# Performance work log

Measured on AMD Instinct MI355X. Metric: run time of the kernel, lower is better.

## Reference

```python
import jax, jax.numpy as jnp
import numpy as np
import math

D = 2048
NH = 16       # query heads
NKV = 4       # kv heads (GQA)
HD = 128
SOFTCLAMP = 50.0
ROPE_BASE = 10000.0
B = 4
SQ_VLM = 1024
SQ_ACT = 64
S_CACHE = 256


def _heads(x, n):
    # [B,S,n*HD] -> [B,n,S,HD]
    b, s, _ = x.shape
    return x.reshape(b, s, n, HD).transpose(0, 2, 1, 3)


def _rope_cos_sin(pos):
    # pos: [B,S] int -> cos,sin [B,1,S,HD]
    inv_freq = 1.0 / (ROPE_BASE ** (jnp.arange(0, HD, 2, dtype=jnp.float32) / HD))
    freqs = pos.astype(jnp.float32)[..., None] * inv_freq  # [B,S,HD/2]
    emb = jnp.concatenate([freqs, freqs], axis=-1)         # [B,S,HD]
    return jnp.cos(emb)[:, None], jnp.sin(emb)[:, None]


def _apply_rope(x, cos, sin):
    # x: [B,H,S,HD]
    x1, x2 = x[..., : HD // 2], x[..., HD // 2 :]
    rot = jnp.concatenate([-x2, x1], axis=-1)
    return x * cos + rot * sin


def setup_inputs() -> dict:
    key = jax.random.key(0)
    ks = jax.random.split(key, 16)
    sc = lambda d: 1.0 / math.sqrt(d)
    inp = {
        'attention_mask': jnp.zeros((B, 1, SQ_VLM + SQ_ACT, S_CACHE + SQ_VLM + SQ_ACT), jnp.float32),
        'pos_vlm': jnp.broadcast_to(jnp.arange(S_CACHE, S_CACHE + SQ_VLM, dtype=jnp.int32), (B, SQ_VLM)),
        'pos_action': jnp.broadcast_to(jnp.arange(S_CACHE + SQ_VLM, S_CACHE + SQ_VLM + SQ_ACT, dtype=jnp.int32), (B, SQ_ACT)),
        'h_vlm': jax.random.normal(ks[0], (B, SQ_VLM, D), jnp.float32),
        'h_action': jax.random.normal(ks[1], (B, SQ_ACT, D), jnp.float32),
        'k_cache': jax.random.normal(ks[2], (B, NKV, S_CACHE, HD), jnp.float32),
        'v_cache': jax.random.normal(ks[3], (B, NKV, S_CACHE, HD), jnp.float32),
        'Wq_vlm': jax.random.normal(ks[4], (D, NH * HD), jnp.float32) * sc(D),
        'Wk_vlm': jax.random.normal(ks[5], (D, NKV * HD), jnp.float32) * sc(D),
        'Wv_vlm': jax.random.normal(ks[6], (D, NKV * HD), jnp.float32) * sc(D),
        'Wq_act': jax.random.normal(ks[7], (D, NH * HD), jnp.float32) * sc(D),
        'Wk_act': jax.random.normal(ks[8], (D, NKV * HD), jnp.float32) * sc(D),
        'Wv_act': jax.random.normal(ks[9], (D, NKV * HD), jnp.float32) * sc(D),
        'Wo_act': jax.random.normal(ks[10], (NH * HD, D), jnp.float32) * sc(NH * HD),
    }
    return inp


def reference(attention_mask, pos_vlm, pos_action, h_vlm, h_action, k_cache, v_cache,
              Wq_vlm, Wk_vlm, Wv_vlm, Wq_act, Wk_act, Wv_act, Wo_act):
    group = NH // NKV

    def qkv(h, pos, Wq, Wk, Wv):
        q = _heads(h @ Wq, NH)
        k = _heads(h @ Wk, NKV)
        v = _heads(h @ Wv, NKV)
        cos, sin = _rope_cos_sin(pos)
        return _apply_rope(q, cos, sin), _apply_rope(k, cos, sin), v

    q_v, k_v, v_v = qkv(h_vlm, pos_vlm, Wq_vlm, Wk_vlm, Wv_vlm)
    q_a, k_a, v_a = qkv(h_action, pos_action, Wq_act, Wk_act, Wv_act)

    # repeat_kv (GQA) on every KV source, cached mixture first (append_non_active order)
    rep = lambda t: jnp.repeat(t, group, axis=1)  # [B,NKV,S,HD] -> [B,NH,S,HD]
    k = jnp.concatenate([rep(k_cache), rep(k_v), rep(k_a)], axis=2)
    v = jnp.concatenate([rep(v_cache), rep(v_v), rep(v_a)], axis=2)
    q = jnp.concatenate([q_v, q_a], axis=2)  # [B,NH,Sq,HD]

    scores = jnp.einsum('bhqd,bhkd->bhqk', q, k) / math.sqrt(HD)
    scores = jnp.tanh(scores / SOFTCLAMP) * SOFTCLAMP + attention_mask
    w = jax.nn.softmax(scores.astype(jnp.float32), axis=-1).astype(q.dtype)
    out = jnp.einsum('bhqk,bhkd->bhqd', w, v)
    out = out.transpose(0, 2, 1, 3).reshape(B, SQ_VLM + SQ_ACT, NH * HD)

    # split by q_lens; 'vlm' is in post_attn_skip_names -> no o_proj, dropped
    out_action = out[:, SQ_VLM:, :]
    return out_action @ Wo_act
```

## Files before the change

### kernel.cpp

```cpp
#include <hip/hip_runtime.h>
#include <cmath>

#define NH 16
#define NKV 4
#define HD 128
#define DMODEL 2048
#define BB 4
#define SQV 1024
#define SQA 64
#define SCACHE 256
#define STOT 1344
#define SQTOT 1088
#define NSPLIT 7

typedef unsigned short u16;
typedef __attribute__((ext_vector_type(8))) short short8;
typedef __attribute__((ext_vector_type(4))) float f32x4;

__device__ __forceinline__ float b2f(u16 u) {
    union { float f; unsigned int i; } x; x.i = ((unsigned int)u) << 16; return x.f;
}
__device__ __forceinline__ u16 f2b(float f) {
    unsigned int x = __float_as_uint(f);
    x = x + 0x7fffu + ((x >> 16) & 1u);
    return (u16)(x >> 16);
}

__device__ __forceinline__ void gload16(const void* g, void* l) {
    __builtin_amdgcn_global_load_lds((const __attribute__((address_space(1))) void*)g,
                                     (__attribute__((address_space(3))) void*)l, 16, 0, 0);
}

__device__ __forceinline__ void transpose_body(const float* in, u16* out, int N,
                                               int bx, int by) {
    __shared__ __align__(16) u16 t[64 * 66];
    int n0 = bx * 64, k0 = by * 64;
    int tid = threadIdx.x;
    int r = tid >> 3;
    int c8 = (tid & 7) * 8;
#pragma unroll
    for (int h = 0; h < 2; h++) {
        int k = r + h * 32;
        const float* f = in + (size_t)(k0 + k) * N + n0 + c8;
        float4 a = *(const float4*)f, b = *(const float4*)(f + 4);
        u16 vv[8] = {f2b(a.x), f2b(a.y), f2b(a.z), f2b(a.w),
                     f2b(b.x), f2b(b.y), f2b(b.z), f2b(b.w)};
#pragma unroll
        for (int j = 0; j < 8; j++) t[(c8 + j) * 66 + k] = vv[j];
    }
    __syncthreads();
#pragma unroll
    for (int h = 0; h < 2; h++) {
        int n = r + h * 32;
        short8 v;
#pragma unroll
        for (int j = 0; j < 8; j++) ((u16*)&v)[j] = t[n * 66 + c8 + j];
        *(short8*)(out + (size_t)(n0 + n) * 2048 + k0 + c8) = v;
    }
}

__device__ __forceinline__ void transpose_vc(const float* vc, u16* VT, int idx) {
    __shared__ __align__(16) u16 tv[64 * 66];
    int bkv = idx >> 3, t8 = idx & 7;
    int key0 = (t8 >> 1) * 64, d0 = (t8 & 1) * 64;
    const float* in = vc + ((size_t)bkv * SCACHE + key0) * HD + d0;
    u16* out = VT + ((size_t)bkv * HD + d0) * STOT + key0;
    int tid = threadIdx.x;
    int r = tid >> 3, c8 = (tid & 7) * 8;
#pragma unroll
    for (int h = 0; h < 2; h++) {
        int k = r + h * 32;
        const float* f = in + (size_t)k * HD + c8;
        float4 a = *(const float4*)f, b = *(const float4*)(f + 4);
        u16 vv[8] = {f2b(a.x), f2b(a.y), f2b(a.z), f2b(a.w),
                     f2b(b.x), f2b(b.y), f2b(b.z), f2b(b.w)};
#pragma unroll
        for (int j = 0; j < 8; j++) tv[(c8 + j) * 66 + k] = vv[j];
    }
    __syncthreads();
#pragma unroll
    for (int h = 0; h < 2; h++) {
        int d = r + h * 32;
        short8 v;
#pragma unroll
        for (int j = 0; j < 8; j++) ((u16*)&v)[j] = tv[d * 66 + c8 + j];
        *(short8*)(out + (size_t)d * STOT + c8) = v;
    }
}

__global__ void k_prep(const float* __restrict__ mask,
                       const float* __restrict__ kc, const float* __restrict__ vc,
                       const float* __restrict__ hv, const float* __restrict__ ha,
                       const float* __restrict__ w0, u16* __restrict__ o0,
                       const float* __restrict__ w1, u16* __restrict__ o1,
                       const float* __restrict__ w2, u16* __restrict__ o2,
                       const float* __restrict__ w3, u16* __restrict__ o3,
                       const float* __restrict__ w4, u16* __restrict__ o4,
                       const float* __restrict__ w5, u16* __restrict__ o5,
                       float* __restrict__ cosT, float* __restrict__ sinT,
                       u16* __restrict__ maskS, u16* __restrict__ K_all, u16* __restrict__ VT_all,
                       u16* __restrict__ hv16, u16* __restrict__ ha16) {
    int gx = blockIdx.x, tid = threadIdx.x;
    if (gx < 3072) {
        if (gx < 256)        transpose_body(w0, o0, 512,  gx & 7,  gx >> 3);
        else if (gx < 512)   { int g = gx - 256;  transpose_body(w1, o1, 512,  g & 7,  g >> 3); }
        else if (gx < 768)   { int g = gx - 512;  transpose_body(w2, o2, 512,  g & 7,  g >> 3); }
        else if (gx < 1024)  { int g = gx - 768;  transpose_body(w3, o3, 512,  g & 7,  g >> 3); }
        else if (gx < 2048)  { int g = gx - 1024; transpose_body(w4, o4, 2048, g & 31, g >> 5); }
        else                 { int g = gx - 2048; transpose_body(w5, o5, 2048, g & 31, g >> 5); }
        return;
    }
    int bx = gx - 3072;
    if (bx < 336) {
        int i = bx * 256 + tid;
        if (i < STOT * 64) {
            int p = i >> 6, j = i & 63;
            float inv = __expf(-(float)j * (9.210340371976184f / 64.0f));
            float ang = (float)p * inv;
            cosT[i] = cosf(ang);
            sinT[i] = sinf(ang);
        }
    } else if (bx < 1680) {
        int i = (bx - 336) * 256 + tid;
        int b = i / (SQA * STOT);
        int r = i % (SQA * STOT);
        size_t s = (size_t)b * SQTOT * STOT + (size_t)SQV * STOT + r;
        maskS[i] = f2b(mask[s]);
    } else if (bx < 1936) {
        int i = (bx - 1680) * 256 + tid;
        int e = i * 8;
        int bk = e / (SCACHE * HD);
        int off = e % (SCACHE * HD);
        size_t dst = (size_t)bk * STOT * HD + off;
        const float* fk = kc + e;
        u16 tk[8];
#pragma unroll
        for (int j = 0; j < 8; j++) tk[j] = f2b(fk[j]);
        *(short8*)(K_all + dst) = *(short8*)tk;
    } else if (bx < 6032) {
        int i = (bx - 1936) * 256 + tid;
        int e = i * 8;
        const float* f = hv + e;
        float4 a = *(const float4*)f, b = *(const float4*)(f + 4);
        u16 t[8] = {f2b(a.x), f2b(a.y), f2b(a.z), f2b(a.w),
                    f2b(b.x), f2b(b.y), f2b(b.z), f2b(b.w)};
        *(short8*)(hv16 + e) = *(short8*)t;
    } else if (bx < 6288) {
        int i = (bx - 6032) * 256 + tid;
        int e = i * 8;
        const float* f = ha + e;
        float4 a = *(const float4*)f, b = *(const float4*)(f + 4);
        u16 t[8] = {f2b(a.x), f2b(a.y), f2b(a.z), f2b(a.w),
                    f2b(b.x), f2b(b.y), f2b(b.z), f2b(b.w)};
        *(short8*)(ha16 + e) = *(short8*)t;
    } else {
        transpose_vc(vc, VT_all, bx - 6288);
    }
}

__global__ __launch_bounds__(256) void k_gemm_qkv(
    const u16* __restrict__ Avlm, const u16* __restrict__ Aact,
    const u16* __restrict__ WkvT, const u16* __restrict__ WvvT,
    const u16* __restrict__ WqaT, const u16* __restrict__ WkaT, const u16* __restrict__ WvaT,
    const int* __restrict__ pos_vlm, const int* __restrict__ pos_act,
    const float* __restrict__ cosT, const float* __restrict__ sinT,
    u16* __restrict__ Qbuf, u16* __restrict__ K_all, u16* __restrict__ VT_all) {
    __shared__ __align__(16) u16 smem[3 * 12288];
    int tid = threadIdx.x;
    int w = tid >> 6, lane = tid & 63;
    int la = lane & 15, lg = lane >> 4;
    int wm = (w & 1) * 32;
    int c2 = w >> 1;
    int ntab[4] = {c2 * 2, c2 * 2 + 1, c2 * 2 + 4, c2 * 2 + 5};

    const u16* A; const u16* Bt; int m0, n0;
    int path;
    int head;
    int bid = blockIdx.x;
    if (bid < 512) {
        m0 = (bid & 63) * 64;
        int yy = bid >> 6;
        path = (yy < 4) ? 0 : 1;
        head = yy & 3;
        n0 = head * 128;
        A = Avlm;
        Bt = (path == 0) ? WkvT : WvvT;
    } else {
        int g = bid - 512;
        m0 = (g & 3) * 64;
        int ny = g >> 2;
        A = Aact;
        if (ny < 16)      { path = 2; head = ny;      Bt = WqaT; n0 = ny * 128; }
        else if (ny < 20) { path = 3; head = ny - 16; Bt = WkaT; n0 = (ny - 16) * 128; }
        else              { path = 4; head = ny - 20; Bt = WvaT; n0 = (ny - 20) * 128; }
    }

    f32x4 acc[2][4];
#pragma unroll
    for (int i = 0; i < 2; i++)
#pragma unroll
        for (int j = 0; j < 4; j++) acc[i][j] = (f32x4){0.f, 0.f, 0.f, 0.f};

    int srow = tid >> 3;
    int scsrc = (((tid & 7) * 16) ^ ((srow & 7) << 4)) >> 1;

#define STAGE_QKV(BASE, KB) do {                                                      \
        u16* Ab_ = (BASE);                                                            \
        u16* Bb_ = Ab_ + 4096;                                                        \
        _Pragma("unroll")                                                             \
        for (int h = 0; h < 2; h++)                                                   \
            gload16(A + (size_t)(m0 + srow + h * 32) * DMODEL + (KB) + scsrc,         \
                    Ab_ + h * 2048 + tid * 8);                                        \
        _Pragma("unroll")                                                             \
        for (int h = 0; h < 4; h++)                                                   \
            gload16(Bt + (size_t)(n0 + srow + h * 32) * DMODEL + (KB) + scsrc,        \
                    Bb_ + h * 2048 + tid * 8);                                        \
    } while (0)

    STAGE_QKV(smem, 0);
    STAGE_QKV(smem + 12288, 64);
    int bufR = 0, bufS = 2;
    int swr = (la & 7) << 3;
    for (int t = 0; t < 32; ++t) {
        if (t < 31) asm volatile("s_waitcnt vmcnt(6)" ::: "memory");
        else        asm volatile("s_waitcnt vmcnt(0)" ::: "memory");
        __builtin_amdgcn_s_barrier();
        asm volatile("" ::: "memory");
        if (t < 30) STAGE_QKV(smem + bufS * 12288, (t + 2) * 64);
        const u16* Ac = smem + bufR * 12288;
        const u16* Bc = Ac + 4096;
#pragma unroll
        for (int kk = 0; kk < 2; kk++) {
            short8 af[2], bf[4];
            int cc = (kk * 32 + lg * 8) ^ swr;
#pragma unroll
            for (int mt = 0; mt < 2; mt++)
                af[mt] = *(const short8*)&Ac[(wm + mt * 16 + la) * 64 + cc];
#pragma unroll
            for (int nt = 0; nt < 4; nt++)
                bf[nt] = *(const short8*)&Bc[(ntab[nt] * 16 + la) * 64 + cc];
#pragma unroll
            for (int mt = 0; mt < 2; mt++)
#pragma unroll
                for (int nt = 0; nt < 4; nt++)
                    acc[mt][nt] = __builtin_amdgcn_mfma_f32_16x16x32_bf16(af[mt], bf[nt], acc[mt][nt], 0, 0, 0);
        }
        bufR = (bufR == 2) ? 0 : bufR + 1;
        bufS = (bufS == 2) ? 0 : bufS + 1;
    }
#undef STAGE_QKV

#pragma unroll
    for (int mt = 0; mt < 2; mt++) {
#pragma unroll
        for (int r = 0; r < 4; r++) {
            int gm = m0 + wm + mt * 16 + lg * 4 + r;
            if (path <= 1) {
                int b = gm >> 10, s = gm & 1023;
                if (path == 0) {
                    size_t base = ((size_t)(b * NKV + head) * STOT + SCACHE + s) * HD;
                    int pos = pos_vlm[gm];
#pragma unroll
                    for (int i = 0; i < 2; i++) {
                        int dlo = ntab[i] * 16 + la;
                        float x1 = acc[mt][i][r], x2 = acc[mt][i + 2][r];
                        float cs = cosT[pos * 64 + dlo], sn = sinT[pos * 64 + dlo];
                        K_all[base + dlo]      = f2b(x1 * cs - x2 * sn);
                        K_all[base + dlo + 64] = f2b(x2 * cs + x1 * sn);
                    }
                } else {
                    size_t vt = ((size_t)(b * NKV + head) * HD) * STOT + SCACHE + s;
#pragma unroll
                    for (int i = 0; i < 4; i++) {
                        int d = ntab[i] * 16 + la;
                        VT_all[vt + (size_t)d * STOT] = f2b(acc[mt][i][r]);
                    }
                }
            } else {
                int b = gm >> 6, s = gm & 63;
                if (path == 2) {
                    int pos = pos_act[gm];
                    size_t qb = ((size_t)(b * NH + head) * SQA + s) * HD;
#pragma unroll
                    for (int i = 0; i < 2; i++) {
                        int dlo = ntab[i] * 16 + la;
                        float x1 = acc[mt][i][r], x2 = acc[mt][i + 2][r];
                        float cs = cosT[pos * 64 + dlo], sn = sinT[pos * 64 + dlo];
                        Qbuf[qb + dlo]      = f2b(x1 * cs - x2 * sn);
                        Qbuf[qb + dlo + 64] = f2b(x2 * cs + x1 * sn);
                    }
                } else if (path == 3) {
                    int pos = pos_act[gm];
                    size_t base = ((size_t)(b * NKV + head) * STOT + SCACHE + SQV + s) * HD;
#pragma unroll
                    for (int i = 0; i < 2; i++) {
                        int dlo = ntab[i] * 16 + la;
                        float x1 = acc[mt][i][r], x2 = acc[mt][i + 2][r];
                        float cs = cosT[pos * 64 + dlo], sn = sinT[pos * 64 + dlo];
                        K_all[base + dlo]      = f2b(x1 * cs - x2 * sn);
                        K_all[base + dlo + 64] = f2b(x2 * cs + x1 * sn);
                    }
                } else {
                    size_t vt = ((size_t)(b * NKV + head) * HD) * STOT + SCACHE + SQV + s;
#pragma unroll
                    for (int i = 0; i < 4; i++) {
                        int d = ntab[i] * 16 + la;
                        VT_all[vt + (size_t)d * STOT] = f2b(acc[mt][i][r]);
                    }
                }
            }
        }
    }
}

__global__ __launch_bounds__(256) void k_attn_split(
    const u16* __restrict__ Qbuf, const u16* __restrict__ K_all, const u16* __restrict__ VT_all,
    const u16* __restrict__ maskS, u16* __restrict__ po, float* __restrict__ pml) {
    int h = blockIdx.x, b = blockIdx.y, p = blockIdx.z;
    int bh = b * NH + h;
    int kvh = h >> 2;
    const u16* Kb  = K_all  + (size_t)(b * NKV + kvh) * STOT * HD;
    const u16* VTb = VT_all + (size_t)(b * NKV + kvh) * HD * STOT;
    const u16* Qb  = Qbuf + (size_t)bh * SQA * HD;
    int tid = threadIdx.x, w = tid >> 6, lane = tid & 63;
    int la = lane & 15, lg = lane >> 4;
    __shared__ __align__(16) u16 Ks[2][64 * 128];
    __shared__ __align__(16) u16 Vt[2][128 * 64];
    __shared__ __align__(16) u16 Ps[4][16 * 72];

    int kr = tid >> 4;
    int ksw = (((tid & 15) * 16) ^ ((kr & 7) << 4)) >> 1;
    int vr = tid >> 3;
    int vsw = (((tid & 7) * 16) ^ ((vr & 7) << 4)) >> 1;

#define ASTAGE(CB, G) do {                                                            \
        _Pragma("unroll")                                                             \
        for (int hh = 0; hh < 4; hh++)                                                \
            gload16(Kb + (size_t)((G) * 64 + kr + hh * 16) * HD + ksw,                \
                    &Ks[CB][hh * 2048 + tid * 8]);                                    \
        _Pragma("unroll")                                                             \
        for (int hh = 0; hh < 4; hh++)                                                \
            gload16(VTb + (size_t)(vr + hh * 32) * STOT + (G) * 64 + vsw,             \
                    &Vt[CB][hh * 2048 + tid * 8]);                                    \
    } while (0)

    ASTAGE(0, p * 3);
    short8 qf[4];
#pragma unroll
    for (int kk = 0; kk < 4; kk++)
        qf[kk] = *(const short8*)(Qb + (size_t)(w * 16 + la) * HD + kk * 32 + lg * 8);
    f32x4 o_acc[8];
#pragma unroll
    for (int nt = 0; nt < 8; nt++) o_acc[nt] = (f32x4){0.f, 0.f, 0.f, 0.f};
    float m_run[4], l_run[4];
#pragma unroll
    for (int r = 0; r < 4; r++) { m_run[r] = -3e38f; l_run[r] = 0.f; }

    int cur = 0;
    int swr = (la & 7) << 3;
    const float scl = 0.08838834764831845f;
    for (int c = 0; c < 3; c++) {
        int g = p * 3 + c;
        u16 mreg[4][4];
#pragma unroll
        for (int nt = 0; nt < 4; nt++)
#pragma unroll
            for (int r = 0; r < 4; r++)
                mreg[nt][r] = maskS[((size_t)(b * SQA + w * 16 + lg * 4 + r)) * STOT +
                                    g * 64 + nt * 16 + la];
        if (c < 2) {
            ASTAGE(cur ^ 1, g + 1);
            asm volatile("s_waitcnt vmcnt(8)" ::: "memory");
        } else {
            asm volatile("s_waitcnt vmcnt(0)" ::: "memory");
        }
        __builtin_amdgcn_s_barrier();
        asm volatile("" ::: "memory");
        f32x4 s_acc[4];
#pragma unroll
        for (int nt = 0; nt < 4; nt++) s_acc[nt] = (f32x4){0.f, 0.f, 0.f, 0.f};
        __builtin_amdgcn_s_setprio(1);
#pragma unroll
        for (int kk = 0; kk < 4; kk++) {
            int cc = (kk * 32 + lg * 8) ^ swr;
#pragma unroll
            for (int nt = 0; nt < 4; nt++) {
                short8 kf = *(const short8*)&Ks[cur][(nt * 16 + la) * 128 + cc];
                s_acc[nt] = __builtin_amdgcn_mfma_f32_16x16x32_bf16(qf[kk], kf, s_acc[nt], 0, 0, 0);
            }
        }
        __builtin_amdgcn_s_setprio(0);
        float sc[4][4];
#pragma unroll
        for (int nt = 0; nt < 4; nt++) {
#pragma unroll
            for (int r = 0; r < 4; r++) {
                float sv = s_acc[nt][r] * scl;
                float x = sv * 0.02f;
                float t = __expf(-2.0f * fabsf(x));
                float th = __fdividef(1.0f - t, 1.0f + t);
                sv = copysignf(th, x) * 50.0f;
                sv += b2f(mreg[nt][r]);
                sc[nt][r] = sv;
            }
        }
#pragma unroll
        for (int r = 0; r < 4; r++) {
            float mx = fmaxf(fmaxf(sc[0][r], sc[1][r]), fmaxf(sc[2][r], sc[3][r]));
#pragma unroll
            for (int sh = 1; sh < 16; sh <<= 1) mx = fmaxf(mx, __shfl_xor(mx, sh, 64));
            if (mx > m_run[r] + 8.0f) {
                float alpha = __expf(m_run[r] - mx);
                m_run[r] = mx;
                l_run[r] *= alpha;
#pragma unroll
                for (int nt = 0; nt < 8; nt++) o_acc[nt][r] *= alpha;
            }
            float rowsum = 0.f;
#pragma unroll
            for (int nt = 0; nt < 4; nt++) {
                float pv = __expf(sc[nt][r] - m_run[r]);
                Ps[w][(lg * 4 + r) * 72 + nt * 16 + la] = f2b(pv);
                rowsum += pv;
            }
#pragma unroll
            for (int sh = 1; sh < 16; sh <<= 1) rowsum += __shfl_xor(rowsum, sh, 64);
            l_run[r] += rowsum;
        }
        __builtin_amdgcn_s_setprio(1);
#pragma unroll
        for (int kk = 0; kk < 2; kk++) {
            short8 pf = *(const short8*)&Ps[w][la * 72 + kk * 32 + lg * 8];
            int cc = (kk * 32 + lg * 8) ^ swr;
#pragma unroll
            for (int nt = 0; nt < 8; nt++) {
                short8 vf = *(const short8*)&Vt[cur][(nt * 16 + la) * 64 + cc];
                o_acc[nt] = __builtin_amdgcn_mfma_f32_16x16x32_bf16(pf, vf, o_acc[nt], 0, 0, 0);
            }
        }
        __builtin_amdgcn_s_setprio(0);
        __builtin_amdgcn_s_barrier();
        cur ^= 1;
    }
#undef ASTAGE
#pragma unroll
    for (int nt = 0; nt < 8; nt++) {
#pragma unroll
        for (int r = 0; r < 4; r++) {
            int sq = w * 16 + lg * 4 + r;
            po[(((size_t)p * 64 + bh) * 64 + sq) * 128 + nt * 16 + la] = f2b(o_acc[nt][r]);
        }
    }
    if (la == 0) {
#pragma unroll
        for (int r = 0; r < 4; r++) {
            int sq = w * 16 + lg * 4 + r;
            size_t mlb = (((size_t)p * 64 + bh) * 64 + sq) * 2;
            pml[mlb] = m_run[r];
            pml[mlb + 1] = l_run[r];
        }
    }
}

__global__ __launch_bounds__(256) void k_attn_red(
    const u16* __restrict__ po, const float* __restrict__ pml, u16* __restrict__ AO) {
    int h = blockIdx.x, b = blockIdx.y, qz = blockIdx.z * 16;
    int bh = b * NH + h;
    __shared__ float wgt[NSPLIT][16];
    int tid = threadIdx.x;
    if (tid < 16) {
        int q = qz + tid;
        float m[NSPLIT], l[NSPLIT], M = -3e38f;
#pragma unroll
        for (int p = 0; p < NSPLIT; p++) {
            size_t mlb = (((size_t)p * 64 + bh) * 64 + q) * 2;
            m[p] = pml[mlb]; l[p] = pml[mlb + 1];
            M = fmaxf(M, m[p]);
        }
        float L = 0.f;
#pragma unroll
        for (int p = 0; p < NSPLIT; p++) L += l[p] * __expf(m[p] - M);
        float inv = 1.0f / L;
#pragma unroll
        for (int p = 0; p < NSPLIT; p++) wgt[p][tid] = __expf(m[p] - M) * inv;
    }
    __syncthreads();
    for (int e = tid; e < 16 * 128; e += 256) {
        int q = qz + (e >> 7), d = e & 127;
        float s = 0.f;
#pragma unroll
        for (int p = 0; p < NSPLIT; p++)
            s += b2f(po[(((size_t)p * 64 + bh) * 64 + q) * 128 + d]) * wgt[p][e >> 7];
        AO[((size_t)(b * SQA + q)) * 2048 + h * HD + d] = f2b(s);
    }
}

__global__ __launch_bounds__(256) void k_gemm_out(
    const u16* __restrict__ A, const u16* __restrict__ WoT, float* __restrict__ out) {
    __shared__ __align__(16) u16 smem[2 * 6144];
    int m0 = blockIdx.x * 32, n0 = blockIdx.y * 64;
    int tid = threadIdx.x;
    int w = tid >> 6, lane = tid & 63;
    int la = lane & 15, lg = lane >> 4;
    int wm = (w & 1) * 16, wn = (w >> 1) * 32;
    f32x4 acc[2];
#pragma unroll
    for (int j = 0; j < 2; j++) acc[j] = (f32x4){0.f, 0.f, 0.f, 0.f};

    int srow = tid >> 3;
    int scsrc = (((tid & 7) * 16) ^ ((srow & 7) << 4)) >> 1;

#define STAGE_OUT(CB, KB) do {                                                        \
        u16* Ab_ = smem + (CB) * 6144;                                                \
        u16* Bb_ = Ab_ + 2048;                                                        \
        gload16(A + (size_t)(m0 + srow) * DMODEL + (KB) + scsrc, Ab_ + tid * 8);      \
        _Pragma("unroll")                                                             \
        for (int h = 0; h < 2; h++)                                                   \
            gload16(WoT + (size_t)(n0 + srow + h * 32) * DMODEL + (KB) + scsrc,       \
                    Bb_ + h * 2048 + tid * 8);                                        \
    } while (0)

    STAGE_OUT(0, 0);
    int cur = 0;
    int swr = (la & 7) << 3;
    for (int kb = 0; kb < DMODEL; kb += 64) {
        if (kb + 64 < DMODEL) {
            STAGE_OUT(cur ^ 1, kb + 64);
            asm volatile("s_waitcnt vmcnt(3)" ::: "memory");
        } else {
            asm volatile("s_waitcnt vmcnt(0)" ::: "memory");
        }
        __builtin_amdgcn_s_barrier();
        asm volatile("" ::: "memory");
        const u16* Ac = smem + cur * 6144;
        const u16* Bc = Ac + 2048;
#pragma unroll
        for (int kk = 0; kk < 2; kk++) {
            int cc = (kk * 32 + lg * 8) ^ swr;
            short8 af = *(const short8*)&Ac[(wm + la) * 64 + cc];
            short8 bf[2];
#pragma unroll
            for (int nt = 0; nt < 2; nt++) bf[nt] = *(const short8*)&Bc[(wn + nt * 16 + la) * 64 + cc];
#pragma unroll
            for (int nt = 0; nt < 2; nt++)
                acc[nt] = __builtin_amdgcn_mfma_f32_16x16x32_bf16(af, bf[nt], acc[nt], 0, 0, 0);
        }
        __builtin_amdgcn_s_barrier();
        cur ^= 1;
    }
#undef STAGE_OUT

#pragma unroll
    for (int r = 0; r < 4; r++) {
        int gm = m0 + wm + lg * 4 + r;
#pragma unroll
        for (int nt = 0; nt < 2; nt++)
            out[(size_t)gm * DMODEL + n0 + wn + nt * 16 + la] = acc[nt][r];
    }
}

extern "C" void kernel_launch(void* const* d_in, const int* in_sizes, int n_in,
                              void* d_out, int out_size, void* d_ws, size_t ws_size,
                              hipStream_t stream) {
    (void)in_sizes; (void)n_in; (void)out_size;
    const float* mask    = (const float*)d_in[0];
    const int*   pos_vlm = (const int*)d_in[1];
    const int*   pos_act = (const int*)d_in[2];
    const float* h_vlm   = (const float*)d_in[3];
    const float* h_act   = (const float*)d_in[4];
    const float* k_cache = (const float*)d_in[5];
    const float* v_cache = (const float*)d_in[6];
    const float* Wk_vlm  = (const float*)d_in[8];
    const float* Wv_vlm  = (const float*)d_in[9];
    const float* Wq_act  = (const float*)d_in[10];
    const float* Wk_act  = (const float*)d_in[11];
    const float* Wv_act  = (const float*)d_in[12];
    const float* Wo_act  = (const float*)d_in[13];

    const size_t NEED = 65273856;
    if (ws_size < NEED) return;
    char* ws = (char*)d_ws;
    float* cosT  = (float*)(ws + 0);
    float* sinT  = (float*)(ws + 344064);
    u16* K_all   = (u16*)(ws + 688128);
    u16* VT_all  = (u16*)(ws + 6193152);
    u16* Qbuf    = (u16*)(ws + 11698176);
    u16* AO      = (u16*)(ws + 12746752);
    u16* WkvT    = (u16*)(ws + 13795328);
    u16* WvvT    = (u16*)(ws + 15892480);
    u16* WqaT    = (u16*)(ws + 17989632);
    u16* WkaT    = (u16*)(ws + 26378240);
    u16* WvaT    = (u16*)(ws + 28475392);
    u16* WoT     = (u16*)(ws + 30572544);
    u16* po      = (u16*)(ws + 38961152);
    float* pml   = (float*)(ws + 46301184);
    u16* maskS   = (u16*)(ws + 46759936);
    u16* hv16    = (u16*)(ws + 47448064);
    u16* ha16    = (u16*)(ws + 64225280);

    hipLaunchKernelGGL(k_prep, dim3(9488), dim3(256), 0, stream,
                       mask, k_cache, v_cache, h_vlm, h_act,
                       Wk_vlm, WkvT, Wv_vlm, WvvT, Wk_act, WkaT, Wv_act, WvaT,
                       Wq_act, WqaT, Wo_act, WoT,
                       cosT, sinT, maskS, K_all, VT_all, hv16, ha16);
    hipLaunchKernelGGL(k_gemm_qkv, dim3(608), dim3(256), 0, stream,
                       hv16, ha16, WkvT, WvvT, WqaT, WkaT, WvaT,
                       pos_vlm, pos_act, cosT, sinT, Qbuf, K_all, VT_all);
    hipLaunchKernelGGL(k_attn_split, dim3(16, 4, NSPLIT), dim3(256), 0, stream,
                       Qbuf, K_all, VT_all, maskS, po, pml);
    hipLaunchKernelGGL(k_attn_red, dim3(16, 4, 4), dim3(256), 0, stream, po, pml, AO);
    hipLaunchKernelGGL(k_gemm_out, dim3(8, 32), dim3(256), 0, stream, AO, WoT, (float*)d_out);
}
```

Measured before the change: 234.4 us.

## Fuse all stages into one cooperative persistent kernel with grid syncs

```diff
diff --git a/kernel.cpp b/kernel.cpp
--- a/kernel.cpp
+++ b/kernel.cpp
@@ -1,5 +1,8 @@
 #include <hip/hip_runtime.h>
+#include <hip/hip_cooperative_groups.h>
 #include <cmath>
+
+namespace cg = cooperative_groups;
 
 #define NH 16
 #define NKV 4
@@ -31,9 +34,24 @@
                                      (__attribute__((address_space(3))) void*)l, 16, 0, 0);
 }
 
-__device__ __forceinline__ void transpose_body(const float* in, u16* out, int N,
+struct MegaArgs {
+    const float *mask, *kc, *vc, *hv, *ha;
+    const float *w0; u16* o0;
+    const float *w1; u16* o1;
+    const float *w2; u16* o2;
+    const float *w3; u16* o3;
+    const float *w4; u16* o4;
+    const float *w5; u16* o5;
+    const int *pos_vlm, *pos_act;
+    float *cosT, *sinT;
+    u16 *maskS, *K_all, *VT_all, *hv16, *ha16, *Qbuf, *po;
+    float* pml;
+    u16* AO;
+    float* out;
+};
+
+__device__ __forceinline__ void transpose_body(u16* t, const float* in, u16* out, int N,
                                                int bx, int by) {
-    __shared__ __align__(16) u16 t[64 * 66];
     int n0 = bx * 64, k0 = by * 64;
     int tid = threadIdx.x;
     int r = tid >> 3;
@@ -59,8 +77,7 @@
     }
 }
 
-__device__ __forceinline__ void transpose_vc(const float* vc, u16* VT, int idx) {
-    __shared__ __align__(16) u16 tv[64 * 66];
+__device__ __forceinline__ void transpose_vc(u16* tv, const float* vc, u16* VT, int idx) {
     int bkv = idx >> 3, t8 = idx & 7;
     int key0 = (t8 >> 1) * 64, d0 = (t8 & 1) * 64;
     const float* in = vc + ((size_t)bkv * SCACHE + key0) * HD + d0;
@@ -88,26 +105,15 @@
     }
 }
 
-__global__ void k_prep(const float* __restrict__ mask,
-                       const float* __restrict__ kc, const float* __restrict__ vc,
-                       const float* __restrict__ hv, const float* __restrict__ ha,
-                       const float* __restrict__ w0, u16* __restrict__ o0,
-                       const float* __restrict__ w1, u16* __restrict__ o1,
-                       const float* __restrict__ w2, u16* __restrict__ o2,
-                       const float* __restrict__ w3, u16* __restrict__ o3,
-                       const float* __restrict__ w4, u16* __restrict__ o4,
-                       const float* __restrict__ w5, u16* __restrict__ o5,
-                       float* __restrict__ cosT, float* __restrict__ sinT,
-                       u16* __restrict__ maskS, u16* __restrict__ K_all, u16* __restrict__ VT_all,
-                       u16* __restrict__ hv16, u16* __restrict__ ha16) {
-    int gx = blockIdx.x, tid = threadIdx.x;
+__device__ __forceinline__ void prep_work(const MegaArgs& a, u16* L, int gx) {
+    int tid = threadIdx.x;
     if (gx < 3072) {
-        if (gx < 256)        transpose_body(w0, o0, 512,  gx & 7,  gx >> 3);
-        else if (gx < 512)   { int g = gx - 256;  transpose_body(w1, o1, 512,  g & 7,  g >> 3); }
-        else if (gx < 768)   { int g = gx - 512;  transpose_body(w2, o2, 512,  g & 7,  g >> 3); }
-        else if (gx < 1024)  { int g = gx - 768;  transpose_body(w3, o3, 512,  g & 7,  g >> 3); }
-        else if (gx < 2048)  { int g = gx - 1024; transpose_body(w4, o4, 2048, g & 31, g >> 5); }
-        else                 { int g = gx - 2048; transpose_body(w5, o5, 2048, g & 31, g >> 5); }
+        if (gx < 256)        transpose_body(L, a.w0, a.o0, 512,  gx & 7,  gx >> 3);
+        else if (gx < 512)   { int g = gx - 256;  transpose_body(L, a.w1, a.o1, 512,  g & 7,  g >> 3); }
+        else if (gx < 768)   { int g = gx - 512;  transpose_body(L, a.w2, a.o2, 512,  g & 7,  g >> 3); }
+        else if (gx < 1024)  { int g = gx - 768;  transpose_body(L, a.w3, a.o3, 512,  g & 7,  g >> 3); }
+        else if (gx < 2048)  { int g = gx - 1024; transpose_body(L, a.w4, a.o4, 2048, g & 31, g >> 5); }
+        else                 { int g = gx - 2048; transpose_body(L, a.w5, a.o5, 2048, g & 31, g >> 5); }
         return;
     }
     int bx = gx - 3072;
@@ -117,55 +123,50 @@
             int p = i >> 6, j = i & 63;
             float inv = __expf(-(float)j * (9.210340371976184f / 64.0f));
             float ang = (float)p * inv;
-            cosT[i] = cosf(ang);
-            sinT[i] = sinf(ang);
+            a.cosT[i] = cosf(ang);
+            a.sinT[i] = sinf(ang);
         }
     } else if (bx < 1680) {
         int i = (bx - 336) * 256 + tid;
         int b = i / (SQA * STOT);
         int r = i % (SQA * STOT);
         size_t s = (size_t)b * SQTOT * STOT + (size_t)SQV * STOT + r;
-        maskS[i] = f2b(mask[s]);
+        a.maskS[i] = f2b(a.mask[s]);
     } else if (bx < 1936) {
         int i = (bx - 1680) * 256 + tid;
         int e = i * 8;
         int bk = e / (SCACHE * HD);
         int off = e % (SCACHE * HD);
         size_t dst = (size_t)bk * STOT * HD + off;
-        const float* fk = kc + e;
+        const float* fk = a.kc + e;
         u16 tk[8];
 #pragma unroll
         for (int j = 0; j < 8; j++) tk[j] = f2b(fk[j]);
-        *(short8*)(K_all + dst) = *(short8*)tk;
+        *(short8*)(a.K_all + dst) = *(short8*)tk;
     } else if (bx < 6032) {
         int i = (bx - 1936) * 256 + tid;
         int e = i * 8;
-        const float* f = hv + e;
-        float4 a = *(const float4*)f, b = *(const float4*)(f + 4);
-        u16 t[8] = {f2b(a.x), f2b(a.y), f2b(a.z), f2b(a.w),
-                    f2b(b.x), f2b(b.y), f2b(b.z), f2b(b.w)};
-        *(short8*)(hv16 + e) = *(short8*)t;
+        const float* f = a.hv + e;
+        float4 p0 = *(const float4*)f, p1 = *(const float4*)(f + 4);
+        u16 t8[8] = {f2b(p0.x), f2b(p0.y), f2b(p0.z), f2b(p0.w),
+                     f2b(p1.x), f2b(p1.y), f2b(p1.z), f2b(p1.w)};
+        *(short8*)(a.hv16 + e) = *(short8*)t8;
     } else if (bx < 6288) {
         int i = (bx - 6032) * 256 + tid;
         int e = i * 8;
-        const float* f = ha + e;
-        float4 a = *(const float4*)f, b = *(const float4*)(f + 4);
-        u16 t[8] = {f2b(a.x), f2b(a.y), f2b(a.z), f2b(a.w),
-                    f2b(b.x), f2b(b.y), f2b(b.z), f2b(b.w)};
-        *(short8*)(ha16 + e) = *(short8*)t;
+        const float* f = a.ha + e;
+        float4 p0 = *(const float4*)f, p1 = *(const float4*)(f + 4);
+        u16 t8[8] = {f2b(p0.x), f2b(p0.y), f2b(p0.z), f2b(p0.w),
+                     f2b(p1.x), f2b(p1.y), f2b(p1.z), f2b(p1.w)};
+        *(short8*)(a.ha16 + e) = *(short8*)t8;
     } else {
-        transpose_vc(vc, VT_all, bx - 6288);
-    }
-}
-
-__global__ __launch_bounds__(256) void k_gemm_qkv(
-    const u16* __restrict__ Avlm, const u16* __restrict__ Aact,
-    const u16* __restrict__ WkvT, const u16* __restrict__ WvvT,
-    const u16* __restrict__ WqaT, const u16* __restrict__ WkaT, const u16* __restrict__ WvaT,
-    const int* __restrict__ pos_vlm, const int* __restrict__ pos_act,
-    const float* __restrict__ cosT, const float* __restrict__ sinT,
-    u16* __restrict__ Qbuf, u16* __restrict__ K_all, u16* __restrict__ VT_all) {
-    __shared__ __align__(16) u16 smem[3 * 12288];
+        transpose_vc(L, a.vc, a.VT_all, bx - 6288);
+    }
+}
+
+__device__ __forceinline__ void qkv_tile(const MegaArgs& a, u16* smem,
+                                         const u16* A, const u16* Bt,
+                                         int m0, int n0, int path, int head) {
     int tid = threadIdx.x;
     int w = tid >> 6, lane = tid & 63;
     int la = lane & 15, lg = lane >> 4;
@@ -173,28 +174,6 @@
     int c2 = w >> 1;
     int ntab[4] = {c2 * 2, c2 * 2 + 1, c2 * 2 + 4, c2 * 2 + 5};
 
-    const u16* A; const u16* Bt; int m0, n0;
-    int path;
-    int head;
-    int bid = blockIdx.x;
-    if (bid < 512) {
-        m0 = (bid & 63) * 64;
-        int yy = bid >> 6;
-        path = (yy < 4) ? 0 : 1;
-        head = yy & 3;
-        n0 = head * 128;
-        A = Avlm;
-        Bt = (path == 0) ? WkvT : WvvT;
-    } else {
-        int g = bid - 512;
-        m0 = (g & 3) * 64;
-        int ny = g >> 2;
-        A = Aact;
-        if (ny < 16)      { path = 2; head = ny;      Bt = WqaT; n0 = ny * 128; }
-        else if (ny < 20) { path = 3; head = ny - 16; Bt = WkaT; n0 = (ny - 16) * 128; }
-        else              { path = 4; head = ny - 20; Bt = WvaT; n0 = (ny - 20) * 128; }
-    }
-
     f32x4 acc[2][4];
 #pragma unroll
     for (int i = 0; i < 2; i++)
@@ -204,8 +183,8 @@
     int srow = tid >> 3;
     int scsrc = (((tid & 7) * 16) ^ ((srow & 7) << 4)) >> 1;
 
-#define STAGE_QKV(BASE, KB) do {                                                      \
-        u16* Ab_ = (BASE);                                                            \
+#define STAGE_QKV(CB, KB) do {                                                        \
+        u16* Ab_ = smem + (CB) * 12288;                                               \
         u16* Bb_ = Ab_ + 4096;                                                        \
         _Pragma("unroll")                                                             \
         for (int h = 0; h < 2; h++)                                                   \
@@ -217,17 +196,19 @@
                     Bb_ + h * 2048 + tid * 8);                                        \
     } while (0)
 
-    STAGE_QKV(smem, 0);
-    STAGE_QKV(smem + 12288, 64);
-    int bufR = 0, bufS = 2;
+    STAGE_QKV(0, 0);
+    int cur = 0;
     int swr = (la & 7) << 3;
-    for (int t = 0; t < 32; ++t) {
-        if (t < 31) asm volatile("s_waitcnt vmcnt(6)" ::: "memory");
-        else        asm volatile("s_waitcnt vmcnt(0)" ::: "memory");
+    for (int kb = 0; kb < DMODEL; kb += 64) {
+        if (kb + 64 < DMODEL) {
+            STAGE_QKV(cur ^ 1, kb + 64);
+            asm volatile("s_waitcnt vmcnt(6)" ::: "memory");
+        } else {
+            asm volatile("s_waitcnt vmcnt(0)" ::: "memory");
+        }
         __builtin_amdgcn_s_barrier();
         asm volatile("" ::: "memory");
-        if (t < 30) STAGE_QKV(smem + bufS * 12288, (t + 2) * 64);
-        const u16* Ac = smem + bufR * 12288;
+        const u16* Ac = smem + cur * 12288;
         const u16* Bc = Ac + 4096;
 #pragma unroll
         for (int kk = 0; kk < 2; kk++) {
@@ -245,8 +226,8 @@
                 for (int nt = 0; nt < 4; nt++)
                     acc[mt][nt] = __builtin_amdgcn_mfma_f32_16x16x32_bf16(af[mt], bf[nt], acc[mt][nt], 0, 0, 0);
         }
-        bufR = (bufR == 2) ? 0 : bufR + 1;
-        bufS = (bufS == 2) ? 0 : bufS + 1;
+        __builtin_amdgcn_s_barrier();
+        cur ^= 1;
     }
 #undef STAGE_QKV
 
@@ -259,53 +240,53 @@
                 int b = gm >> 10, s = gm & 1023;
                 if (path == 0) {
                     size_t base = ((size_t)(b * NKV + head) * STOT + SCACHE + s) * HD;
-                    int pos = pos_vlm[gm];
+                    int pos = a.pos_vlm[gm];
 #pragma unroll
                     for (int i = 0; i < 2; i++) {
                         int dlo = ntab[i] * 16 + la;
                         float x1 = acc[mt][i][r], x2 = acc[mt][i + 2][r];
-                        float cs = cosT[pos * 64 + dlo], sn = sinT[pos * 64 + dlo];
-                        K_all[base + dlo]      = f2b(x1 * cs - x2 * sn);
-                        K_all[base + dlo + 64] = f2b(x2 * cs + x1 * sn);
+                        float cs = a.cosT[pos * 64 + dlo], sn = a.sinT[pos * 64 + dlo];
+                        a.K_all[base + dlo]      = f2b(x1 * cs - x2 * sn);
+                        a.K_all[base + dlo + 64] = f2b(x2 * cs + x1 * sn);
                     }
                 } else {
                     size_t vt = ((size_t)(b * NKV + head) * HD) * STOT + SCACHE + s;
 #pragma unroll
                     for (int i = 0; i < 4; i++) {
                         int d = ntab[i] * 16 + la;
-                        VT_all[vt + (size_t)d * STOT] = f2b(acc[mt][i][r]);
+                        a.VT_all[vt + (size_t)d * STOT] = f2b(acc[mt][i][r]);
                     }
                 }
             } else {
                 int b = gm >> 6, s = gm & 63;
                 if (path == 2) {
-                    int pos = pos_act[gm];
+                    int pos = a.pos_act[gm];
                     size_t qb = ((size_t)(b * NH + head) * SQA + s) * HD;
 #pragma unroll
                     for (int i = 0; i < 2; i++) {
                         int dlo = ntab[i] * 16 + la;
                         float x1 = acc[mt][i][r], x2 = acc[mt][i + 2][r];
-                        float cs = cosT[pos * 64 + dlo], sn = sinT[pos * 64 + dlo];
-                        Qbuf[qb + dlo]      = f2b(x1 * cs - x2 * sn);
-                        Qbuf[qb + dlo + 64] = f2b(x2 * cs + x1 * sn);
+                        float cs = a.cosT[pos * 64 + dlo], sn = a.sinT[pos * 64 + dlo];
+                        a.Qbuf[qb + dlo]      = f2b(x1 * cs - x2 * sn);
+                        a.Qbuf[qb + dlo + 64] = f2b(x2 * cs + x1 * sn);
                     }
                 } else if (path == 3) {
-                    int pos = pos_act[gm];
+                    int pos = a.pos_act[gm];
                     size_t base = ((size_t)(b * NKV + head) * STOT + SCACHE + SQV + s) * HD;
 #pragma unroll
                     for (int i = 0; i < 2; i++) {
                         int dlo = ntab[i] * 16 + la;
                         float x1 = acc[mt][i][r], x2 = acc[mt][i + 2][r];
-                        float cs = cosT[pos * 64 + dlo], sn = sinT[pos * 64 + dlo];
-                        K_all[base + dlo]      = f2b(x1 * cs - x2 * sn);
-                        K_all[base + dlo + 64] = f2b(x2 * cs + x1 * sn);
+                        float cs = a.cosT[pos * 64 + dlo], sn = a.sinT[pos * 64 + dlo];
+                        a.K_all[base + dlo]      = f2b(x1 * cs - x2 * sn);
+                        a.K_all[base + dlo + 64] = f2b(x2 * cs + x1 * sn);
                     }
                 } else {
                     size_t vt = ((size_t)(b * NKV + head) * HD) * STOT + SCACHE + SQV + s;
 #pragma unroll
                     for (int i = 0; i < 4; i++) {
                         int d = ntab[i] * 16 + la;
-                        VT_all[vt + (size_t)d * STOT] = f2b(acc[mt][i][r]);
+                        a.VT_all[vt + (size_t)d * STOT] = f2b(acc[mt][i][r]);
                     }
                 }
             }
@@ -313,38 +294,55 @@
     }
 }
 
-__global__ __launch_bounds__(256) void k_attn_split(
-    const u16* __restrict__ Qbuf, const u16* __restrict__ K_all, const u16* __restrict__ VT_all,
-    const u16* __restrict__ maskS, u16* __restrict__ po, float* __restrict__ pml) {
-    int h = blockIdx.x, b = blockIdx.y, p = blockIdx.z;
+__device__ __forceinline__ void qkv_work(const MegaArgs& a, u16* smem, int bid) {
+    if (bid < 512) {
+        int m0 = (bid & 63) * 64;
+        int yy = bid >> 6;
+        int path = (yy < 4) ? 0 : 1;
+        int head = yy & 3;
+        qkv_tile(a, smem, a.hv16, (path == 0) ? a.o0 : a.o1, m0, head * 128, path, head);
+    } else {
+        int g = bid - 512;
+        int m0 = (g & 3) * 64;
+        int ny = g >> 2;
+        int path, head, n0; const u16* Bt;
+        if (ny < 16)      { path = 2; head = ny;      Bt = a.o4; n0 = ny * 128; }
+        else if (ny < 20) { path = 3; head = ny - 16; Bt = a.o2; n0 = (ny - 16) * 128; }
+        else              { path = 4; head = ny - 20; Bt = a.o3; n0 = (ny - 20) * 128; }
+        qkv_tile(a, smem, a.ha16, Bt, m0, n0, path, head);
+    }
+}
+
+__device__ __forceinline__ void attn_work(const MegaArgs& a, u16* LDS, int bid) {
+    int h = bid & 15, b = (bid >> 4) & 3, p = bid >> 6;
     int bh = b * NH + h;
     int kvh = h >> 2;
-    const u16* Kb  = K_all  + (size_t)(b * NKV + kvh) * STOT * HD;
-    const u16* VTb = VT_all + (size_t)(b * NKV + kvh) * HD * STOT;
-    const u16* Qb  = Qbuf + (size_t)bh * SQA * HD;
+    const u16* Kb  = a.K_all  + (size_t)(b * NKV + kvh) * STOT * HD;
+    const u16* VTb = a.VT_all + (size_t)(b * NKV + kvh) * HD * STOT;
+    const u16* Qb  = a.Qbuf + (size_t)bh * SQA * HD;
     int tid = threadIdx.x, w = tid >> 6, lane = tid & 63;
     int la = lane & 15, lg = lane >> 4;
-    __shared__ __align__(16) u16 Ks[2][64 * 128];
-    __shared__ __align__(16) u16 Vt[2][128 * 64];
-    __shared__ __align__(16) u16 Ps[4][16 * 72];
+    u16* Ks = LDS;
+    u16* Vt = LDS + 8192;
+    u16* Ps = LDS + 16384;
 
     int kr = tid >> 4;
     int ksw = (((tid & 15) * 16) ^ ((kr & 7) << 4)) >> 1;
     int vr = tid >> 3;
     int vsw = (((tid & 7) * 16) ^ ((vr & 7) << 4)) >> 1;
 
-#define ASTAGE(CB, G) do {                                                            \
+#define ASTG(G) do {                                                                  \
         _Pragma("unroll")                                                             \
         for (int hh = 0; hh < 4; hh++)                                                \
             gload16(Kb + (size_t)((G) * 64 + kr + hh * 16) * HD + ksw,                \
-                    &Ks[CB][hh * 2048 + tid * 8]);                                    \
+                    &Ks[hh * 2048 + tid * 8]);                                        \
         _Pragma("unroll")                                                             \
         for (int hh = 0; hh < 4; hh++)                                                \
             gload16(VTb + (size_t)(vr + hh * 32) * STOT + (G) * 64 + vsw,             \
-                    &Vt[CB][hh * 2048 + tid * 8]);                                    \
+                    &Vt[hh * 2048 + tid * 8]);                                        \
     } while (0)
 
-    ASTAGE(0, p * 3);
+    ASTG(p * 3);
     short8 qf[4];
 #pragma unroll
     for (int kk = 0; kk < 4; kk++)
@@ -356,7 +354,6 @@
 #pragma unroll
     for (int r = 0; r < 4; r++) { m_run[r] = -3e38f; l_run[r] = 0.f; }
 
-    int cur = 0;
     int swr = (la & 7) << 3;
     const float scl = 0.08838834764831845f;
     for (int c = 0; c < 3; c++) {
@@ -366,14 +363,9 @@
         for (int nt = 0; nt < 4; nt++)
 #pragma unroll
             for (int r = 0; r < 4; r++)
-                mreg[nt][r] = maskS[((size_t)(b * SQA + w * 16 + lg * 4 + r)) * STOT +
-                                    g * 64 + nt * 16 + la];
-        if (c < 2) {
-            ASTAGE(cur ^ 1, g + 1);
-            asm volatile("s_waitcnt vmcnt(8)" ::: "memory");
-        } else {
-            asm volatile("s_waitcnt vmcnt(0)" ::: "memory");
-        }
+                mreg[nt][r] = a.maskS[((size_t)(b * SQA + w * 16 + lg * 4 + r)) * STOT +
+                                      g * 64 + nt * 16 + la];
+        asm volatile("s_waitcnt vmcnt(0)" ::: "memory");
         __builtin_amdgcn_s_barrier();
         asm volatile("" ::: "memory");
         f32x4 s_acc[4];
@@ -385,7 +377,7 @@
             int cc = (kk * 32 + lg * 8) ^ swr;
 #pragma unroll
             for (int nt = 0; nt < 4; nt++) {
-                short8 kf = *(const short8*)&Ks[cur][(nt * 16 + la) * 128 + cc];
+                short8 kf = *(const short8*)&Ks[(nt * 16 + la) * 128 + cc];
                 s_acc[nt] = __builtin_amdgcn_mfma_f32_16x16x32_bf16(qf[kk], kf, s_acc[nt], 0, 0, 0);
             }
         }
@@ -420,7 +412,7 @@
 #pragma unroll
             for (int nt = 0; nt < 4; nt++) {
                 float pv = __expf(sc[nt][r] - m_run[r]);
-                Ps[w][(lg * 4 + r) * 72 + nt * 16 + la] = f2b(pv);
+                Ps[w * 1152 + (lg * 4 + r) * 72 + nt * 16 + la] = f2b(pv);
                 rowsum += pv;
             }
 #pragma unroll
@@ -430,25 +422,25 @@
         __builtin_amdgcn_s_setprio(1);
 #pragma unroll
         for (int kk = 0; kk < 2; kk++) {
-            short8 pf = *(const short8*)&Ps[w][la * 72 + kk * 32 + lg * 8];
+            short8 pf = *(const short8*)&Ps[w * 1152 + la * 72 + kk * 32 + lg * 8];
             int cc = (kk * 32 + lg * 8) ^ swr;
 #pragma unroll
             for (int nt = 0; nt < 8; nt++) {
-                short8 vf = *(const short8*)&Vt[cur][(nt * 16 + la) * 64 + cc];
+                short8 vf = *(const short8*)&Vt[(nt * 16 + la) * 64 + cc];
                 o_acc[nt] = __builtin_amdgcn_mfma_f32_16x16x32_bf16(pf, vf, o_acc[nt], 0, 0, 0);
             }
         }
         __builtin_amdgcn_s_setprio(0);
         __builtin_amdgcn_s_barrier();
-        cur ^= 1;
-    }
-#undef ASTAGE
+        if (c < 2) ASTG(g + 1);
+    }
+#undef ASTG
 #pragma unroll
     for (int nt = 0; nt < 8; nt++) {
 #pragma unroll
         for (int r = 0; r < 4; r++) {
             int sq = w * 16 + lg * 4 + r;
-            po[(((size_t)p * 64 + bh) * 64 + sq) * 128 + nt * 16 + la] = f2b(o_acc[nt][r]);
+            a.po[(((size_t)p * 64 + bh) * 64 + sq) * 128 + nt * 16 + la] = f2b(o_acc[nt][r]);
         }
     }
     if (la == 0) {
@@ -456,17 +448,15 @@
         for (int r = 0; r < 4; r++) {
             int sq = w * 16 + lg * 4 + r;
             size_t mlb = (((size_t)p * 64 + bh) * 64 + sq) * 2;
-            pml[mlb] = m_run[r];
-            pml[mlb + 1] = l_run[r];
-        }
-    }
-}
-
-__global__ __launch_bounds__(256) void k_attn_red(
-    const u16* __restrict__ po, const float* __restrict__ pml, u16* __restrict__ AO) {
-    int h = blockIdx.x, b = blockIdx.y, qz = blockIdx.z * 16;
+            a.pml[mlb] = m_run[r];
+            a.pml[mlb + 1] = l_run[r];
+        }
+    }
+}
+
+__device__ __forceinline__ void red_work(const MegaArgs& a, float* wgt, int bid) {
+    int h = bid & 15, b = (bid >> 4) & 3, qz = (bid >> 6) * 16;
     int bh = b * NH + h;
-    __shared__ float wgt[NSPLIT][16];
     int tid = threadIdx.x;
     if (tid < 16) {
         int q = qz + tid;
@@ -474,7 +464,7 @@
 #pragma unroll
         for (int p = 0; p < NSPLIT; p++) {
             size_t mlb = (((size_t)p * 64 + bh) * 64 + q) * 2;
-            m[p] = pml[mlb]; l[p] = pml[mlb + 1];
+            m[p] = a.pml[mlb]; l[p] = a.pml[mlb + 1];
             M = fmaxf(M, m[p]);
         }
         float L = 0.f;
@@ -482,7 +472,7 @@
         for (int p = 0; p < NSPLIT; p++) L += l[p] * __expf(m[p] - M);
         float inv = 1.0f / L;
 #pragma unroll
-        for (int p = 0; p < NSPLIT; p++) wgt[p][tid] = __expf(m[p] - M) * inv;
+        for (int p = 0; p < NSPLIT; p++) wgt[p * 16 + tid] = __expf(m[p] - M) * inv;
     }
     __syncthreads();
     for (int e = tid; e < 16 * 128; e += 256) {
@@ -490,15 +480,13 @@
         float s = 0.f;
 #pragma unroll
         for (int p = 0; p < NSPLIT; p++)
-            s += b2f(po[(((size_t)p * 64 + bh) * 64 + q) * 128 + d]) * wgt[p][e >> 7];
-        AO[((size_t)(b * SQA + q)) * 2048 + h * HD + d] = f2b(s);
-    }
-}
-
-__global__ __launch_bounds__(256) void k_gemm_out(
-    const u16* __restrict__ A, const u16* __restrict__ WoT, float* __restrict__ out) {
-    __shared__ __align__(16) u16 smem[2 * 6144];
-    int m0 = blockIdx.x * 32, n0 = blockIdx.y * 64;
+            s += b2f(a.po[(((size_t)p * 64 + bh) * 64 + q) * 128 + d]) * wgt[p * 16 + (e >> 7)];
+        a.AO[((size_t)(b * SQA + q)) * 2048 + h * HD + d] = f2b(s);
+    }
+}
+
+__device__ __forceinline__ void out_work(const MegaArgs& a, u16* smem, int bid) {
+    int m0 = (bid & 7) * 32, n0 = (bid >> 3) * 64;
     int tid = threadIdx.x;
     int w = tid >> 6, lane = tid & 63;
     int la = lane & 15, lg = lane >> 4;
@@ -513,10 +501,10 @@
 #define STAGE_OUT(CB, KB) do {                                                        \
         u16* Ab_ = smem + (CB) * 6144;                                                \
         u16* Bb_ = Ab_ + 2048;                                                        \
-        gload16(A + (size_t)(m0 + srow) * DMODEL + (KB) + scsrc, Ab_ + tid * 8);      \
+        gload16(a.AO + (size_t)(m0 + srow) * DMODEL + (KB) + scsrc, Ab_ + tid * 8);   \
         _Pragma("unroll")                                                             \
         for (int h = 0; h < 2; h++)                                                   \
-            gload16(WoT + (size_t)(n0 + srow + h * 32) * DMODEL + (KB) + scsrc,       \
+            gload16(a.o5 + (size_t)(n0 + srow + h * 32) * DMODEL + (KB) + scsrc,      \
                     Bb_ + h * 2048 + tid * 8);                                        \
     } while (0)
 
@@ -555,59 +543,109 @@
         int gm = m0 + wm + lg * 4 + r;
 #pragma unroll
         for (int nt = 0; nt < 2; nt++)
-            out[(size_t)gm * DMODEL + n0 + wn + nt * 16 + la] = acc[nt][r];
-    }
+            a.out[(size_t)gm * DMODEL + n0 + wn + nt * 16 + la] = acc[nt][r];
+    }
+}
+
+__global__ __launch_bounds__(256, 2) void k_mega(MegaArgs a) {
+    __shared__ __align__(16) u16 SMEM[24576];
+    cg::grid_group grid = cg::this_grid();
+    int b0 = blockIdx.x;
+
+    for (int gx = b0; gx < 9488; gx += 512) {
+        __syncthreads();
+        prep_work(a, SMEM, gx);
+    }
+    grid.sync();
+
+    qkv_work(a, SMEM, b0);
+    if (b0 % 5 == 2 && b0 / 5 < 96) {
+        __syncthreads();
+        qkv_work(a, SMEM, 512 + b0 / 5);
+    }
+    grid.sync();
+
+    if (b0 < 448) attn_work(a, SMEM, b0);
+    grid.sync();
+
+    if (b0 < 256) red_work(a, (float*)SMEM, b0);
+    grid.sync();
+
+    if (b0 < 256) out_work(a, SMEM, b0);
+}
+
+__global__ __launch_bounds__(256) void k_prep_f(MegaArgs a) {
+    __shared__ __align__(16) u16 L[4224];
+    prep_work(a, L, blockIdx.x);
+}
+__global__ __launch_bounds__(256) void k_qkv_f(MegaArgs a) {
+    __shared__ __align__(16) u16 L[24576];
+    qkv_work(a, L, blockIdx.x);
+}
+__global__ __launch_bounds__(256) void k_attn_f(MegaArgs a) {
+    __shared__ __align__(16) u16 L[20992];
+    attn_work(a, L, blockIdx.x);
+}
+__global__ __launch_bounds__(256) void k_red_f(MegaArgs a) {
+    __shared__ float W[NSPLIT * 16];
+    red_work(a, W, blockIdx.x);
+}
+__global__ __launch_bounds__(256) void k_out_f(MegaArgs a) {
+    __shared__ __align__(16) u16 L[12288];
+    out_work(a, L, blockIdx.x);
 }
 
 extern "C" void kernel_launch(void* const* d_in, const int* in_sizes, int n_in,
                               void* d_out, int out_size, void* d_ws, size_t ws_size,
                               hipStream_t stream) {
     (void)in_sizes; (void)n_in; (void)out_size;
-    const float* mask    = (const float*)d_in[0];
-    const int*   pos_vlm = (const int*)d_in[1];
-    const int*   pos_act = (const int*)d_in[2];
-    const float* h_vlm   = (const float*)d_in[3];
-    const float* h_act   = (const float*)d_in[4];
-    const float* k_cache = (const float*)d_in[5];
-    const float* v_cache = (const float*)d_in[6];
-    const float* Wk_vlm  = (const float*)d_in[8];
-    const float* Wv_vlm  = (const float*)d_in[9];
-    const float* Wq_act  = (const float*)d_in[10];
-    const float* Wk_act  = (const float*)d_in[11];
-    const float* Wv_act  = (const float*)d_in[12];
-    const float* Wo_act  = (const float*)d_in[13];
-
     const size_t NEED = 65273856;
     if (ws_size < NEED) return;
     char* ws = (char*)d_ws;
-    float* cosT  = (float*)(ws + 0);
-    float* sinT  = (float*)(ws + 344064);
-    u16* K_all   = (u16*)(ws + 688128);
-    u16* VT_all  = (u16*)(ws + 6193152);
-    u16* Qbuf    = (u16*)(ws + 11698176);
-    u16* AO      = (u16*)(ws + 12746752);
-    u16* WkvT    = (u16*)(ws + 13795328);
-    u16* WvvT    = (u16*)(ws + 15892480);
-    u16* WqaT    = (u16*)(ws + 17989632);
-    u16* WkaT    = (u16*)(ws + 26378240);
-    u16* WvaT    = (u16*)(ws + 28475392);
-    u16* WoT     = (u16*)(ws + 30572544);
-    u16* po      = (u16*)(ws + 38961152);
-    float* pml   = (float*)(ws + 46301184);
-    u16* maskS   = (u16*)(ws + 46759936);
-    u16* hv16    = (u16*)(ws + 47448064);
-    u16* ha16    = (u16*)(ws + 64225280);
-
-    hipLaunchKernelGGL(k_prep, dim3(9488), dim3(256), 0, stream,
-                       mask, k_cache, v_cache, h_vlm, h_act,
-                       Wk_vlm, WkvT, Wv_vlm, WvvT, Wk_act, WkaT, Wv_act, WvaT,
-                       Wq_act, WqaT, Wo_act, WoT,
-                       cosT, sinT, maskS, K_all, VT_all, hv16, ha16);
-    hipLaunchKernelGGL(k_gemm_qkv, dim3(608), dim3(256), 0, stream,
-                       hv16, ha16, WkvT, WvvT, WqaT, WkaT, WvaT,
-                       pos_vlm, pos_act, cosT, sinT, Qbuf, K_all, VT_all);
-    hipLaunchKernelGGL(k_attn_split, dim3(16, 4, NSPLIT), dim3(256), 0, stream,
-                       Qbuf, K_all, VT_all, maskS, po, pml);
-    hipLaunchKernelGGL(k_attn_red, dim3(16, 4, 4), dim3(256), 0, stream, po, pml, AO);
-    hipLaunchKernelGGL(k_gemm_out, dim3(8, 32), dim3(256), 0, stream, AO, WoT, (float*)d_out);
-}
+
+    MegaArgs a;
+    a.mask    = (const float*)d_in[0];
+    a.pos_vlm = (const int*)d_in[1];
+    a.pos_act = (const int*)d_in[2];
+    a.hv      = (const float*)d_in[3];
+    a.ha      = (const float*)d_in[4];
+    a.kc      = (const float*)d_in[5];
+    a.vc      = (const float*)d_in[6];
+    a.w0 = (const float*)d_in[8];
+    a.w1 = (const float*)d_in[9];
+    a.w2 = (const float*)d_in[11];
+    a.w3 = (const float*)d_in[12];
+    a.w4 = (const float*)d_in[10];
+    a.w5 = (const float*)d_in[13];
+
+    a.cosT  = (float*)(ws + 0);
+    a.sinT  = (float*)(ws + 344064);
+    a.K_all = (u16*)(ws + 688128);
+    a.VT_all= (u16*)(ws + 6193152);
+    a.Qbuf  = (u16*)(ws + 11698176);
+    a.AO    = (u16*)(ws + 12746752);
+    a.o0    = (u16*)(ws + 13795328);
+    a.o1    = (u16*)(ws + 15892480);
+    a.o4    = (u16*)(ws + 17989632);
+    a.o2    = (u16*)(ws + 26378240);
+    a.o3    = (u16*)(ws + 28475392);
+    a.o5    = (u16*)(ws + 30572544);
+    a.po    = (u16*)(ws + 38961152);
+    a.pml   = (float*)(ws + 46301184);
+    a.maskS = (u16*)(ws + 46759936);
+    a.hv16  = (u16*)(ws + 47448064);
+    a.ha16  = (u16*)(ws + 64225280);
+    a.out   = (float*)d_out;
+
+    void* params[] = { &a };
+    hipError_t err = hipLaunchCooperativeKernel(k_mega, dim3(512), dim3(256),
+                                                params, 0, stream);
+    if (err != hipSuccess) {
+        (void)hipGetLastError();
+        hipLaunchKernelGGL(k_prep_f, dim3(9488), dim3(256), 0, stream, a);
+        hipLaunchKernelGGL(k_qkv_f,  dim3(608),  dim3(256), 0, stream, a);
+        hipLaunchKernelGGL(k_attn_f, dim3(448),  dim3(256), 0, stream, a);
+        hipLaunchKernelGGL(k_red_f,  dim3(256),  dim3(256), 0, stream, a);
+        hipLaunchKernelGGL(k_out_f,  dim3(256),  dim3(256), 0, stream, a);
+    }
+}
```

After: 507.1 us. 2.16x slower.
